# Performance work log

Measured on AMD Instinct MI355X. Metric: run time of the kernel, lower is better.

## Reference

```python
import jax, jax.numpy as jnp
import numpy as np

N_NODES = 100000
N_EDGES = 1600000
IN_DIM, HID_DIM, OUT_DIM = 384, 64, 64
DROP_P = 0.5


def setup_inputs() -> dict:
    key = jax.random.key(0)
    ks = jax.random.split(key, 9)
    x = jax.random.normal(ks[0], (N_NODES, IN_DIM), dtype=jnp.float32)
    edge_index = jax.random.randint(ks[1], (2, N_EDGES), 0, N_NODES, dtype=jnp.int64)
    edge_weight = jax.random.uniform(ks[2], (N_EDGES,), dtype=jnp.float32)
    W1 = jax.random.normal(ks[3], (IN_DIM, HID_DIM), dtype=jnp.float32) * (1.0 / np.sqrt(IN_DIM))
    b1 = jnp.zeros((HID_DIM,), dtype=jnp.float32)
    W2 = jax.random.normal(ks[4], (HID_DIM, OUT_DIM), dtype=jnp.float32) * (1.0 / np.sqrt(HID_DIM))
    b2 = jnp.zeros((OUT_DIM,), dtype=jnp.float32)
    drop_mask1 = jax.random.bernoulli(ks[5], 1.0 - DROP_P, (N_NODES, IN_DIM))
    drop_mask2 = jax.random.bernoulli(ks[6], 1.0 - DROP_P, (N_NODES, HID_DIM))
    return {"x": x, "edge_index": edge_index, "edge_weight": edge_weight,
            "W1": W1, "b1": b1, "W2": W2, "b2": b2,
            "drop_mask1": drop_mask1, "drop_mask2": drop_mask2}


def _gcn_conv(h, W, b, src, dst, edge_weight, n_nodes):
    # GCNConv: linear transform first (smaller dim), then normalized sparse aggregation
    h = h @ W                                        # [N, d_out]
    msg = h[src] * edge_weight[:, None]              # gather over edges [E, d_out]
    agg = jax.ops.segment_sum(msg, dst, num_segments=n_nodes)  # scatter-add [N, d_out]
    return agg + b


def reference(x, edge_index, edge_weight, W1, b1, W2, b2, drop_mask1, drop_mask2):
    scale = 1.0 / (1.0 - DROP_P)
    src, dst = edge_index[0], edge_index[1]
    n = x.shape[0]
    h = x * drop_mask1.astype(x.dtype) * scale                  # dropout (training)
    h = jax.nn.relu(_gcn_conv(h, W1, b1, src, dst, edge_weight, n))
    h = h * drop_mask2.astype(h.dtype) * scale                  # dropout (training)
    return _gcn_conv(h, W2, b2, src, dst, edge_weight, n)
```

## Files before the change

kernel.cpp:

```cpp
#include <hip/hip_runtime.h>
#include <hip/hip_bf16.h>
#include <stdint.h>

#define N_NODES 100000
#define N_EDGES 1600000
#define IN_DIM  384
#define HID_DIM 64
#define SCAN_NB 391

typedef __attribute__((ext_vector_type(8))) short short8_t;
typedef __attribute__((ext_vector_type(4))) float f32x4;

__global__ void k_detect(const uint32_t* __restrict__ ei,
                         const uint32_t* __restrict__ m1,
                         int* __restrict__ flags) {
    int l = threadIdx.x;
    uint32_t hi = ei[2 * l + 1];
    int ei64 = __all(hi == 0u);

    uint32_t maxb = 0;
    int bf = 0, f16 = 0, hib = 0;
    for (int i = 0; i < 4; ++i) {
        uint32_t w = m1[l * 4 + i];
        uint32_t b0 = w & 0xffu, b1 = (w >> 8) & 0xffu,
                 b2 = (w >> 16) & 0xffu, b3 = (w >> 24) & 0xffu;
        uint32_t mb = b0 > b1 ? b0 : b1;
        uint32_t mb2 = b2 > b3 ? b2 : b3;
        mb = mb > mb2 ? mb : mb2;
        maxb = maxb > mb ? maxb : mb;
        if ((w & 0xffffu) == 0x3f80u) bf = 1;
        if ((w & 0xffffu) == 0x3c00u) f16 = 1;
        if ((b1 | b2 | b3) != 0u) hib = 1;
    }
    int small  = __all(maxb <= 1u);
    int anybf  = __any(bf);
    int anyf16 = __any(f16);
    int anyhib = __any(hib);
    if (l == 0) {
        flags[0] = ei64;
        int mm;
        if (small)                 mm = anyhib ? 3 : 4;
        else if (anybf || anyf16)  mm = 0;
        else                       mm = 2;
        flags[1] = mm;
    }
}

__device__ __forceinline__ float mask_at(const void* p, int mode, long idx) {
    if (mode == 0) return ((const uint16_t*)p)[idx] ? 2.0f : 0.0f;
    if (mode == 2) return ((const float*)p)[idx] != 0.0f ? 2.0f : 0.0f;
    if (mode == 3) return ((const uint8_t*)p)[idx] ? 2.0f : 0.0f;
    return ((const int*)p)[idx] ? 2.0f : 0.0f;
}

__device__ __forceinline__ void load_edge(const int* p32, int mode64, long e,
                                          int& s, int& d) {
    if (mode64) { s = p32[2 * e]; d = p32[2 * (N_EDGES + e)]; }
    else        { s = p32[e];     d = p32[N_EDGES + e]; }
}

__device__ __forceinline__ ushort f2bf(float f) {
    uint32_t u = __float_as_uint(f);
    return (ushort)((u + 0x7fffu + ((u >> 16) & 1u)) >> 16);
}
__device__ __forceinline__ float bf2f(ushort h) {
    return __uint_as_float(((uint32_t)h) << 16);
}

__global__ __launch_bounds__(256) void k_hist(const void* __restrict__ ei,
                                              uint32_t* __restrict__ deg,
                                              const int* __restrict__ flags) {
    const int mode64 = flags[0];
    const int* p32 = (const int*)ei;
    for (long e = (long)blockIdx.x * 256 + threadIdx.x; e < N_EDGES;
         e += (long)gridDim.x * 256) {
        int s, d; load_edge(p32, mode64, e, s, d);
        atomicAdd(&deg[d], 1u);
    }
}

__global__ __launch_bounds__(256) void k_scanA(const uint32_t* __restrict__ deg,
                                               uint32_t* __restrict__ partials) {
    __shared__ uint32_t sbuf[256];
    int idx = blockIdx.x * 256 + threadIdx.x;
    uint32_t v = idx < N_NODES ? deg[idx] : 0u;
    sbuf[threadIdx.x] = v;
    __syncthreads();
    for (int off = 128; off > 0; off >>= 1) {
        if (threadIdx.x < off) sbuf[threadIdx.x] += sbuf[threadIdx.x + off];
        __syncthreads();
    }
    if (threadIdx.x == 0) partials[blockIdx.x] = sbuf[0];
}

__global__ __launch_bounds__(512) void k_scanB(const uint32_t* __restrict__ partials,
                                               uint32_t* __restrict__ poff,
                                               uint32_t* __restrict__ starts) {
    __shared__ uint32_t sbuf[512];
    int t = threadIdx.x;
    uint32_t v = t < SCAN_NB ? partials[t] : 0u;
    sbuf[t] = v;
    __syncthreads();
    for (int off = 1; off < 512; off <<= 1) {
        uint32_t add = t >= off ? sbuf[t - off] : 0u;
        __syncthreads();
        sbuf[t] += add;
        __syncthreads();
    }
    if (t < SCAN_NB) poff[t] = sbuf[t] - v;
    if (t == SCAN_NB - 1) starts[N_NODES] = sbuf[t];
}

__global__ __launch_bounds__(256) void k_scanC(const uint32_t* __restrict__ deg,
                                               const uint32_t* __restrict__ poff,
                                               uint32_t* __restrict__ starts) {
    __shared__ uint32_t sbuf[256];
    int idx = blockIdx.x * 256 + threadIdx.x;
    uint32_t v = idx < N_NODES ? deg[idx] : 0u;
    sbuf[threadIdx.x] = v;
    __syncthreads();
    for (int off = 1; off < 256; off <<= 1) {
        uint32_t add = threadIdx.x >= off ? sbuf[threadIdx.x - off] : 0u;
        __syncthreads();
        sbuf[threadIdx.x] += add;
        __syncthreads();
    }
    if (idx < N_NODES) starts[idx] = poff[blockIdx.x] + sbuf[threadIdx.x] - v;
}

__global__ __launch_bounds__(256) void k_reorder(const void* __restrict__ ei,
                                                 const float* __restrict__ ew,
                                                 uint32_t* __restrict__ cursors,
                                                 int2* __restrict__ sorted,
                                                 const int* __restrict__ flags) {
    const int mode64 = flags[0];
    const int* p32 = (const int*)ei;
    for (long e = (long)blockIdx.x * 256 + threadIdx.x; e < N_EDGES;
         e += (long)gridDim.x * 256) {
        int s, d; load_edge(p32, mode64, e, s, d);
        float w = ew[e];
        uint32_t pos = atomicAdd(&cursors[d], 1u);
        sorted[pos] = make_int2(s, __float_as_int(w));
    }
}

__global__ __launch_bounds__(256) void k_packW(const float* __restrict__ W1,
                                               ushort* __restrict__ Wpack) {
    const int ks = blockIdx.x;
    const int t  = threadIdx.x;
    const int nt = t >> 6, l = t & 63;
    ushort hs[8], ls[8];
#pragma unroll
    for (int j = 0; j < 8; ++j) {
        float wv = W1[(ks * 32 + (l >> 4) * 8 + j) * 64 + nt * 16 + (l & 15)];
        ushort h = f2bf(wv);
        hs[j] = h;
        ls[j] = f2bf(wv - bf2f(h));
    }
    *(short8_t*)&Wpack[((8 * ks + nt) * 64 + l) * 8]     = *(short8_t*)hs;
    *(short8_t*)&Wpack[((8 * ks + 4 + nt) * 64 + l) * 8] = *(short8_t*)ls;
}

__global__ __launch_bounds__(256) void k1_mfma(
        const float* __restrict__ x, const void* __restrict__ m1,
        const ushort* __restrict__ Wpack, ushort* __restrict__ Hb,
        const int* __restrict__ flags) {
    const int mmode = flags[1];
    const int t = threadIdx.x;
    const int l = t & 63, w = t >> 6;
    const int node0 = blockIdx.x * 64;
    const long row = node0 + w * 16 + (l & 15);
    const int kq = (l >> 4) * 8;
    const bool valid = row < N_NODES;

    f32x4 acc[4];
#pragma unroll
    for (int i = 0; i < 4; ++i) acc[i] = (f32x4)0.0f;

    for (int ks = 0; ks < 12; ++ks) {
        float xv[8];
        if (valid) {
            long gb = row * IN_DIM + ks * 32 + kq;
            float4 x0 = *(const float4*)(x + gb);
            float4 x1 = *(const float4*)(x + gb + 4);
            xv[0] = x0.x; xv[1] = x0.y; xv[2] = x0.z; xv[3] = x0.w;
            xv[4] = x1.x; xv[5] = x1.y; xv[6] = x1.z; xv[7] = x1.w;
            float mv[8];
            if (mmode == 0) {
                const ushort* mp = (const ushort*)m1 + gb;
                ushort4 a = *(const ushort4*)mp;
                ushort4 b = *(const ushort4*)(mp + 4);
                mv[0] = a.x ? 2.f : 0.f; mv[1] = a.y ? 2.f : 0.f;
                mv[2] = a.z ? 2.f : 0.f; mv[3] = a.w ? 2.f : 0.f;
                mv[4] = b.x ? 2.f : 0.f; mv[5] = b.y ? 2.f : 0.f;
                mv[6] = b.z ? 2.f : 0.f; mv[7] = b.w ? 2.f : 0.f;
            } else if (mmode == 2) {
                const float* mp = (const float*)m1 + gb;
                float4 a = *(const float4*)mp;
                float4 b = *(const float4*)(mp + 4);
                mv[0] = a.x != 0.f ? 2.f : 0.f; mv[1] = a.y != 0.f ? 2.f : 0.f;
                mv[2] = a.z != 0.f ? 2.f : 0.f; mv[3] = a.w != 0.f ? 2.f : 0.f;
                mv[4] = b.x != 0.f ? 2.f : 0.f; mv[5] = b.y != 0.f ? 2.f : 0.f;
                mv[6] = b.z != 0.f ? 2.f : 0.f; mv[7] = b.w != 0.f ? 2.f : 0.f;
            } else if (mmode == 3) {
                uint2 mb = *(const uint2*)((const uint8_t*)m1 + gb);
#pragma unroll
                for (int j = 0; j < 4; ++j) {
                    mv[j]     = ((mb.x >> (8 * j)) & 0xffu) ? 2.f : 0.f;
                    mv[4 + j] = ((mb.y >> (8 * j)) & 0xffu) ? 2.f : 0.f;
                }
            } else {
                const int* mp = (const int*)m1 + gb;
                int4 a = *(const int4*)mp;
                int4 b = *(const int4*)(mp + 4);
                mv[0] = a.x ? 2.f : 0.f; mv[1] = a.y ? 2.f : 0.f;
                mv[2] = a.z ? 2.f : 0.f; mv[3] = a.w ? 2.f : 0.f;
                mv[4] = b.x ? 2.f : 0.f; mv[5] = b.y ? 2.f : 0.f;
                mv[6] = b.z ? 2.f : 0.f; mv[7] = b.w ? 2.f : 0.f;
            }
#pragma unroll
            for (int j = 0; j < 8; ++j) xv[j] *= mv[j];
        } else {
#pragma unroll
            for (int j = 0; j < 8; ++j) xv[j] = 0.0f;
        }
        ushort ap[8];
#pragma unroll
        for (int j = 0; j < 8; ++j) ap[j] = f2bf(xv[j]);
        short8_t ah = *(short8_t*)ap;

#pragma unroll
        for (int nt = 0; nt < 4; ++nt) {
            short8_t bh = *(const short8_t*)&Wpack[((8 * ks + nt) * 64 + l) * 8];
            short8_t bl = *(const short8_t*)&Wpack[((8 * ks + 4 + nt) * 64 + l) * 8];
            acc[nt] = __builtin_amdgcn_mfma_f32_16x16x32_bf16(ah, bh, acc[nt], 0, 0, 0);
            acc[nt] = __builtin_amdgcn_mfma_f32_16x16x32_bf16(ah, bl, acc[nt], 0, 0, 0);
        }
    }
    const int r0 = (l >> 4) * 4;
#pragma unroll
    for (int nt = 0; nt < 4; ++nt) {
#pragma unroll
        for (int r = 0; r < 4; ++r) {
            long node = node0 + w * 16 + r0 + r;
            if (node < N_NODES)
                Hb[node * 64 + nt * 16 + (l & 15)] = f2bf(acc[nt][r]);
        }
    }
}

__global__ __launch_bounds__(256) void k_aggmlp(
        const ushort* __restrict__ Hb, const int2* __restrict__ sorted,
        const uint32_t* __restrict__ starts, const float* __restrict__ b1,
        const void* __restrict__ m2, const float* __restrict__ W2,
        ushort* __restrict__ H2b, const int* __restrict__ flags) {
    __shared__ float w2s[64 * 64];
    __shared__ float vbuf[4][64];
    const int mmode = flags[1];
    for (int i = threadIdx.x; i < 4096; i += 256) w2s[i] = W2[i];
    __syncthreads();

    const int lane = threadIdx.x & 63;
    const int w = threadIdx.x >> 6;
    const long n = (long)blockIdx.x * 4 + w;
    uint32_t e  = starts[n];
    uint32_t e1 = starts[n + 1];
    float acc = 0.0f;
    for (; e + 4 <= e1; e += 4) {
        int2 p0 = sorted[e],     p1 = sorted[e + 1];
        int2 p2 = sorted[e + 2], p3 = sorted[e + 3];
        float v0 = bf2f(Hb[(long)p0.x * 64 + lane]);
        float v1 = bf2f(Hb[(long)p1.x * 64 + lane]);
        float v2 = bf2f(Hb[(long)p2.x * 64 + lane]);
        float v3 = bf2f(Hb[(long)p3.x * 64 + lane]);
        acc = fmaf(v0, __int_as_float(p0.y), acc);
        acc = fmaf(v1, __int_as_float(p1.y), acc);
        acc = fmaf(v2, __int_as_float(p2.y), acc);
        acc = fmaf(v3, __int_as_float(p3.y), acc);
    }
    for (; e < e1; ++e) {
        int2 p0 = sorted[e];
        acc = fmaf(bf2f(Hb[(long)p0.x * 64 + lane]), __int_as_float(p0.y), acc);
    }
    float u = acc + b1[lane];
    u = u > 0.0f ? u : 0.0f;
    u *= mask_at(m2, mmode, n * 64 + lane);
    vbuf[w][lane] = u;
    float h2 = 0.0f;
#pragma unroll
    for (int j = 0; j < 64; j += 4) {
        float4 v4 = *(const float4*)&vbuf[w][j];
        h2 = fmaf(v4.x, w2s[(j + 0) * 64 + lane], h2);
        h2 = fmaf(v4.y, w2s[(j + 1) * 64 + lane], h2);
        h2 = fmaf(v4.z, w2s[(j + 2) * 64 + lane], h2);
        h2 = fmaf(v4.w, w2s[(j + 3) * 64 + lane], h2);
    }
    H2b[n * 64 + lane] = f2bf(h2);
}

__global__ __launch_bounds__(256) void k_agg(const ushort* __restrict__ Hb,
                                             const int2* __restrict__ sorted,
                                             const uint32_t* __restrict__ starts,
                                             const float* __restrict__ bias,
                                             float* __restrict__ dest) {
    const int lane = threadIdx.x & 63;
    const long n = (long)blockIdx.x * 4 + (threadIdx.x >> 6);
    if (n >= N_NODES) return;
    uint32_t e  = starts[n];
    uint32_t e1 = starts[n + 1];
    float acc = bias[lane];
    for (; e + 4 <= e1; e += 4) {
        int2 p0 = sorted[e],     p1 = sorted[e + 1];
        int2 p2 = sorted[e + 2], p3 = sorted[e + 3];
        float v0 = bf2f(Hb[(long)p0.x * 64 + lane]);
        float v1 = bf2f(Hb[(long)p1.x * 64 + lane]);
        float v2 = bf2f(Hb[(long)p2.x * 64 + lane]);
        float v3 = bf2f(Hb[(long)p3.x * 64 + lane]);
        acc = fmaf(v0, __int_as_float(p0.y), acc);
        acc = fmaf(v1, __int_as_float(p1.y), acc);
        acc = fmaf(v2, __int_as_float(p2.y), acc);
        acc = fmaf(v3, __int_as_float(p3.y), acc);
    }
    for (; e < e1; ++e) {
        int2 p0 = sorted[e];
        acc = fmaf(bf2f(Hb[(long)p0.x * 64 + lane]), __int_as_float(p0.y), acc);
    }
    dest[n * 64 + lane] = acc;
}

__global__ __launch_bounds__(256) void k_scatter(
        const ushort* __restrict__ Hb, const void* __restrict__ ei,
        const float* __restrict__ ew, float* __restrict__ dest,
        const int* __restrict__ flags) {
    const int mode64 = flags[0];
    const int lane = threadIdx.x & 63;
    const long wid = (long)blockIdx.x * 4 + (threadIdx.x >> 6);
    const long nw = (long)gridDim.x * 4;
    const int* p32 = (const int*)ei;
    for (long e = wid; e < N_EDGES; e += nw) {
        int s, d; load_edge(p32, mode64, e, s, d);
        float w = ew[e];
        float v = bf2f(Hb[(long)s * 64 + lane]) * w;
        atomicAdd(&dest[(long)d * 64 + lane], v);
    }
}

__global__ __launch_bounds__(256) void k3_mlp(
        const float* __restrict__ agg, const float* __restrict__ b1,
        const void* __restrict__ m2, const float* __restrict__ W2,
        ushort* __restrict__ H2b, const int* __restrict__ flags) {
    __shared__ float w2s[64 * 64];
    __shared__ float vbuf[4][64];
    const int mmode = flags[1];
    for (int i = threadIdx.x; i < 4096; i += 256) w2s[i] = W2[i];
    __syncthreads();
    const int lane = threadIdx.x & 63;
    const int w = threadIdx.x >> 6;
    const float bc = b1[lane];
    const long wid = (long)blockIdx.x * 4 + w;
    const long nw = (long)gridDim.x * 4;
    for (long n = wid; n < N_NODES; n += nw) {
        float u = agg[n * 64 + lane] + bc;
        u = u > 0.0f ? u : 0.0f;
        u *= mask_at(m2, mmode, n * 64 + lane);
        vbuf[w][lane] = u;
        float acc = 0.0f;
#pragma unroll
        for (int j = 0; j < 64; j += 4) {
            float4 v4 = *(const float4*)&vbuf[w][j];
            acc = fmaf(v4.x, w2s[(j + 0) * 64 + lane], acc);
            acc = fmaf(v4.y, w2s[(j + 1) * 64 + lane], acc);
            acc = fmaf(v4.z, w2s[(j + 2) * 64 + lane], acc);
            acc = fmaf(v4.w, w2s[(j + 3) * 64 + lane], acc);
        }
        H2b[n * 64 + lane] = f2bf(acc);
    }
}

__global__ void k_init_out(float* __restrict__ out, const float* __restrict__ b2) {
    const long total = (long)N_NODES * 16;
    for (long j = (long)blockIdx.x * 256 + threadIdx.x; j < total;
         j += (long)gridDim.x * 256) {
        ((float4*)out)[j] = ((const float4*)b2)[j & 15];
    }
}

extern "C" void kernel_launch(void* const* d_in, const int* in_sizes, int n_in,
                              void* d_out, int out_size, void* d_ws, size_t ws_size,
                              hipStream_t stream) {
    const float* x  = (const float*)d_in[0];
    const void*  ei = d_in[1];
    const float* ew = (const float*)d_in[2];
    const float* W1 = (const float*)d_in[3];
    const float* b1 = (const float*)d_in[4];
    const float* W2 = (const float*)d_in[5];
    const float* b2 = (const float*)d_in[6];
    const void*  m1 = d_in[7];
    const void*  m2 = d_in[8];
    float* out = (float*)d_out;

    char* ws = (char*)d_ws;
    size_t off = 0;
    auto alloc = [&](size_t bytes) {
        char* p = ws + off;
        off += (bytes + 255) & ~(size_t)255;
        return p;
    };
    int*      flags   = (int*)alloc(32);
    ushort*   Hb      = (ushort*)alloc((size_t)N_NODES * 64 * 2);
    ushort*   H2b     = (ushort*)alloc((size_t)N_NODES * 64 * 2);
    float*    AGG     = (float*)alloc((size_t)N_NODES * 64 * 4);
    int2*     sorted  = (int2*)alloc((size_t)N_EDGES * 8);
    uint32_t* starts  = (uint32_t*)alloc((size_t)(N_NODES + 1) * 4);
    uint32_t* deg     = (uint32_t*)alloc((size_t)N_NODES * 4);
    uint32_t* cursors = (uint32_t*)alloc((size_t)N_NODES * 4);
    uint32_t* poff    = (uint32_t*)alloc((size_t)SCAN_NB * 4);
    ushort*   Wpack   = (ushort*)alloc((size_t)12 * 8 * 64 * 8 * 2);
    size_t need = off;

    hipLaunchKernelGGL(k_detect, dim3(1), dim3(64), 0, stream,
                       (const uint32_t*)ei, (const uint32_t*)m1, flags);
    hipLaunchKernelGGL(k_packW, dim3(12), dim3(256), 0, stream, W1, Wpack);

    if (ws_size >= need) {
        hipMemsetAsync(deg, 0, (size_t)N_NODES * 4, stream);
        hipLaunchKernelGGL(k_hist, dim3(2048), dim3(256), 0, stream,
                           ei, deg, flags);
        hipLaunchKernelGGL(k_scanA, dim3(SCAN_NB), dim3(256), 0, stream,
                           deg, poff);
        hipLaunchKernelGGL(k_scanB, dim3(1), dim3(512), 0, stream,
                           poff, cursors, starts);
        hipLaunchKernelGGL(k_scanC, dim3(SCAN_NB), dim3(256), 0, stream,
                           deg, cursors, starts);
        hipMemcpyAsync(cursors, starts, (size_t)N_NODES * 4,
                       hipMemcpyDeviceToDevice, stream);
        hipLaunchKernelGGL(k_reorder, dim3(2048), dim3(256), 0, stream,
                           ei, ew, cursors, sorted, flags);
        hipLaunchKernelGGL(k1_mfma, dim3((N_NODES + 63) / 64), dim3(256), 0, stream,
                           x, m1, Wpack, Hb, flags);
        hipLaunchKernelGGL(k_aggmlp, dim3(N_NODES / 4), dim3(256), 0, stream,
                           Hb, sorted, starts, b1, m2, W2, H2b, flags);
        hipLaunchKernelGGL(k_agg, dim3(N_NODES / 4), dim3(256), 0, stream,
                           H2b, sorted, starts, b2, out);
    } else {
        hipMemsetAsync(AGG, 0, (size_t)N_NODES * 64 * 4, stream);
        hipLaunchKernelGGL(k1_mfma, dim3((N_NODES + 63) / 64), dim3(256), 0, stream,
                           x, m1, Wpack, Hb, flags);
        hipLaunchKernelGGL(k_scatter, dim3(4096), dim3(256), 0, stream,
                           Hb, ei, ew, AGG, flags);
        hipLaunchKernelGGL(k3_mlp, dim3(1024), dim3(256), 0, stream,
                           AGG, b1, m2, W2, H2b, flags);
        hipLaunchKernelGGL(k_init_out, dim3(2048), dim3(256), 0, stream, out, b2);
        hipLaunchKernelGGL(k_scatter, dim3(4096), dim3(256), 0, stream,
                           H2b, ei, ew, out, flags);
    }
}
```

Before: 785.3 us.

## Partition degree histogram and CSR cursors into eight copies to cut atomic contention

Edges are binned into eight per-partition histograms and cursor arrays, chosen by block index. The scan runs over the combined partition-major array and also writes the cursors directly, which drops the device-to-device memcpy. Each aggregation now walks eight short segments per node and loads sixteen start offsets, with a 2-way unroll instead of 4. This lowers contention on the histogram and reorder atomics, at the cost of scattered small segments and extra index loads in the gather kernels. The CSR buffers now share workspace with the unused fallback AGG buffer.

Result: slower. 855.9 us (+9.0%).

```diff
diff --git a/kernel.cpp b/kernel.cpp
--- a/kernel.cpp
+++ b/kernel.cpp
@@ -6,7 +6,10 @@
 #define N_EDGES 1600000
 #define IN_DIM  384
 #define HID_DIM 64
-#define SCAN_NB 391
+#define NPART   8
+#define NP      (NPART * N_NODES)
+#define SCAN8_NB 782
+#define EGRID   2048
 
 typedef __attribute__((ext_vector_type(8))) short short8_t;
 typedef __attribute__((ext_vector_type(4))) float f32x4;
@@ -67,24 +70,31 @@
     return __uint_as_float(((uint32_t)h) << 16);
 }
 
-__global__ __launch_bounds__(256) void k_hist(const void* __restrict__ ei,
-                                              uint32_t* __restrict__ deg,
-                                              const int* __restrict__ flags) {
+__global__ __launch_bounds__(256) void k_hist8(const void* __restrict__ ei,
+                                               uint32_t* __restrict__ deg8,
+                                               const int* __restrict__ flags) {
     const int mode64 = flags[0];
     const int* p32 = (const int*)ei;
+    const long pbase = (long)(blockIdx.x & (NPART - 1)) * N_NODES;
     for (long e = (long)blockIdx.x * 256 + threadIdx.x; e < N_EDGES;
-         e += (long)gridDim.x * 256) {
+         e += (long)EGRID * 256) {
         int s, d; load_edge(p32, mode64, e, s, d);
-        atomicAdd(&deg[d], 1u);
-    }
-}
-
-__global__ __launch_bounds__(256) void k_scanA(const uint32_t* __restrict__ deg,
-                                               uint32_t* __restrict__ partials) {
+        atomicAdd(&deg8[pbase + d], 1u);
+    }
+}
+
+__global__ __launch_bounds__(256) void k_scanA8(const uint32_t* __restrict__ deg,
+                                                uint32_t* __restrict__ partials) {
     __shared__ uint32_t sbuf[256];
-    int idx = blockIdx.x * 256 + threadIdx.x;
-    uint32_t v = idx < N_NODES ? deg[idx] : 0u;
-    sbuf[threadIdx.x] = v;
+    long base = (long)blockIdx.x * 1024 + threadIdx.x * 4;
+    uint32_t s = 0;
+    if (base + 3 < NP) {
+        uint4 v = *(const uint4*)&deg[base];
+        s = v.x + v.y + v.z + v.w;
+    } else {
+        for (int j = 0; j < 4; ++j) if (base + j < NP) s += deg[base + j];
+    }
+    sbuf[threadIdx.x] = s;
     __syncthreads();
     for (int off = 128; off > 0; off >>= 1) {
         if (threadIdx.x < off) sbuf[threadIdx.x] += sbuf[threadIdx.x + off];
@@ -93,31 +103,39 @@
     if (threadIdx.x == 0) partials[blockIdx.x] = sbuf[0];
 }
 
-__global__ __launch_bounds__(512) void k_scanB(const uint32_t* __restrict__ partials,
-                                               uint32_t* __restrict__ poff,
-                                               uint32_t* __restrict__ starts) {
-    __shared__ uint32_t sbuf[512];
+__global__ __launch_bounds__(1024) void k_scanB8(const uint32_t* __restrict__ partials,
+                                                 uint32_t* __restrict__ poff,
+                                                 uint32_t* __restrict__ starts) {
+    __shared__ uint32_t sbuf[1024];
     int t = threadIdx.x;
-    uint32_t v = t < SCAN_NB ? partials[t] : 0u;
+    uint32_t v = t < SCAN8_NB ? partials[t] : 0u;
     sbuf[t] = v;
     __syncthreads();
-    for (int off = 1; off < 512; off <<= 1) {
+    for (int off = 1; off < 1024; off <<= 1) {
         uint32_t add = t >= off ? sbuf[t - off] : 0u;
         __syncthreads();
         sbuf[t] += add;
         __syncthreads();
     }
-    if (t < SCAN_NB) poff[t] = sbuf[t] - v;
-    if (t == SCAN_NB - 1) starts[N_NODES] = sbuf[t];
-}
-
-__global__ __launch_bounds__(256) void k_scanC(const uint32_t* __restrict__ deg,
-                                               const uint32_t* __restrict__ poff,
-                                               uint32_t* __restrict__ starts) {
+    if (t < SCAN8_NB) poff[t] = sbuf[t] - v;
+    if (t == SCAN8_NB - 1) starts[NP] = sbuf[t];
+}
+
+__global__ __launch_bounds__(256) void k_scanC8(const uint32_t* __restrict__ deg,
+                                                const uint32_t* __restrict__ poff,
+                                                uint32_t* __restrict__ starts,
+                                                uint32_t* __restrict__ cur) {
     __shared__ uint32_t sbuf[256];
-    int idx = blockIdx.x * 256 + threadIdx.x;
-    uint32_t v = idx < N_NODES ? deg[idx] : 0u;
-    sbuf[threadIdx.x] = v;
+    long base = (long)blockIdx.x * 1024 + threadIdx.x * 4;
+    uint32_t v[4] = {0, 0, 0, 0};
+    if (base + 3 < NP) {
+        uint4 q = *(const uint4*)&deg[base];
+        v[0] = q.x; v[1] = q.y; v[2] = q.z; v[3] = q.w;
+    } else {
+        for (int j = 0; j < 4; ++j) if (base + j < NP) v[j] = deg[base + j];
+    }
+    uint32_t ts = v[0] + v[1] + v[2] + v[3];
+    sbuf[threadIdx.x] = ts;
     __syncthreads();
     for (int off = 1; off < 256; off <<= 1) {
         uint32_t add = threadIdx.x >= off ? sbuf[threadIdx.x - off] : 0u;
@@ -125,21 +143,29 @@
         sbuf[threadIdx.x] += add;
         __syncthreads();
     }
-    if (idx < N_NODES) starts[idx] = poff[blockIdx.x] + sbuf[threadIdx.x] - v;
-}
-
-__global__ __launch_bounds__(256) void k_reorder(const void* __restrict__ ei,
-                                                 const float* __restrict__ ew,
-                                                 uint32_t* __restrict__ cursors,
-                                                 int2* __restrict__ sorted,
-                                                 const int* __restrict__ flags) {
+    uint32_t run = poff[blockIdx.x] + sbuf[threadIdx.x] - ts;
+    for (int j = 0; j < 4; ++j) {
+        if (base + j < NP) {
+            starts[base + j] = run;
+            cur[base + j]    = run;
+            run += v[j];
+        }
+    }
+}
+
+__global__ __launch_bounds__(256) void k_reorder8(const void* __restrict__ ei,
+                                                  const float* __restrict__ ew,
+                                                  uint32_t* __restrict__ cur8,
+                                                  int2* __restrict__ sorted,
+                                                  const int* __restrict__ flags) {
     const int mode64 = flags[0];
     const int* p32 = (const int*)ei;
+    const long pbase = (long)(blockIdx.x & (NPART - 1)) * N_NODES;
     for (long e = (long)blockIdx.x * 256 + threadIdx.x; e < N_EDGES;
-         e += (long)gridDim.x * 256) {
+         e += (long)EGRID * 256) {
         int s, d; load_edge(p32, mode64, e, s, d);
         float w = ew[e];
-        uint32_t pos = atomicAdd(&cursors[d], 1u);
+        uint32_t pos = atomicAdd(&cur8[pbase + d], 1u);
         sorted[pos] = make_int2(s, __float_as_int(w));
     }
 }
@@ -249,6 +275,31 @@
     }
 }
 
+__device__ __forceinline__ float agg_node(const ushort* __restrict__ Hb,
+                                          const int2* __restrict__ sorted,
+                                          const uint32_t* __restrict__ starts,
+                                          int n, int lane) {
+    float acc = 0.0f;
+#pragma unroll 1
+    for (int p = 0; p < NPART; ++p) {
+        uint32_t e  = starts[p * N_NODES + n];
+        uint32_t e1 = starts[p * N_NODES + n + 1];
+        for (; e + 2 <= e1; e += 2) {
+            int2 p0 = sorted[e];
+            int2 p1 = sorted[e + 1];
+            float v0 = bf2f(Hb[(long)p0.x * 64 + lane]);
+            float v1 = bf2f(Hb[(long)p1.x * 64 + lane]);
+            acc = fmaf(v0, __int_as_float(p0.y), acc);
+            acc = fmaf(v1, __int_as_float(p1.y), acc);
+        }
+        if (e < e1) {
+            int2 p0 = sorted[e];
+            acc = fmaf(bf2f(Hb[(long)p0.x * 64 + lane]), __int_as_float(p0.y), acc);
+        }
+    }
+    return acc;
+}
+
 __global__ __launch_bounds__(256) void k_aggmlp(
         const ushort* __restrict__ Hb, const int2* __restrict__ sorted,
         const uint32_t* __restrict__ starts, const float* __restrict__ b1,
@@ -262,29 +313,11 @@
 
     const int lane = threadIdx.x & 63;
     const int w = threadIdx.x >> 6;
-    const long n = (long)blockIdx.x * 4 + w;
-    uint32_t e  = starts[n];
-    uint32_t e1 = starts[n + 1];
-    float acc = 0.0f;
-    for (; e + 4 <= e1; e += 4) {
-        int2 p0 = sorted[e],     p1 = sorted[e + 1];
-        int2 p2 = sorted[e + 2], p3 = sorted[e + 3];
-        float v0 = bf2f(Hb[(long)p0.x * 64 + lane]);
-        float v1 = bf2f(Hb[(long)p1.x * 64 + lane]);
-        float v2 = bf2f(Hb[(long)p2.x * 64 + lane]);
-        float v3 = bf2f(Hb[(long)p3.x * 64 + lane]);
-        acc = fmaf(v0, __int_as_float(p0.y), acc);
-        acc = fmaf(v1, __int_as_float(p1.y), acc);
-        acc = fmaf(v2, __int_as_float(p2.y), acc);
-        acc = fmaf(v3, __int_as_float(p3.y), acc);
-    }
-    for (; e < e1; ++e) {
-        int2 p0 = sorted[e];
-        acc = fmaf(bf2f(Hb[(long)p0.x * 64 + lane]), __int_as_float(p0.y), acc);
-    }
+    const int n = blockIdx.x * 4 + w;
+    float acc = agg_node(Hb, sorted, starts, n, lane);
     float u = acc + b1[lane];
     u = u > 0.0f ? u : 0.0f;
-    u *= mask_at(m2, mmode, n * 64 + lane);
+    u *= mask_at(m2, mmode, (long)n * 64 + lane);
     vbuf[w][lane] = u;
     float h2 = 0.0f;
 #pragma unroll
@@ -295,7 +328,7 @@
         h2 = fmaf(v4.z, w2s[(j + 2) * 64 + lane], h2);
         h2 = fmaf(v4.w, w2s[(j + 3) * 64 + lane], h2);
     }
-    H2b[n * 64 + lane] = f2bf(h2);
+    H2b[(long)n * 64 + lane] = f2bf(h2);
 }
 
 __global__ __launch_bounds__(256) void k_agg(const ushort* __restrict__ Hb,
@@ -304,28 +337,10 @@
                                              const float* __restrict__ bias,
                                              float* __restrict__ dest) {
     const int lane = threadIdx.x & 63;
-    const long n = (long)blockIdx.x * 4 + (threadIdx.x >> 6);
+    const int n = blockIdx.x * 4 + (threadIdx.x >> 6);
     if (n >= N_NODES) return;
-    uint32_t e  = starts[n];
-    uint32_t e1 = starts[n + 1];
-    float acc = bias[lane];
-    for (; e + 4 <= e1; e += 4) {
-        int2 p0 = sorted[e],     p1 = sorted[e + 1];
-        int2 p2 = sorted[e + 2], p3 = sorted[e + 3];
-        float v0 = bf2f(Hb[(long)p0.x * 64 + lane]);
-        float v1 = bf2f(Hb[(long)p1.x * 64 + lane]);
-        float v2 = bf2f(Hb[(long)p2.x * 64 + lane]);
-        float v3 = bf2f(Hb[(long)p3.x * 64 + lane]);
-        acc = fmaf(v0, __int_as_float(p0.y), acc);
-        acc = fmaf(v1, __int_as_float(p1.y), acc);
-        acc = fmaf(v2, __int_as_float(p2.y), acc);
-        acc = fmaf(v3, __int_as_float(p3.y), acc);
-    }
-    for (; e < e1; ++e) {
-        int2 p0 = sorted[e];
-        acc = fmaf(bf2f(Hb[(long)p0.x * 64 + lane]), __int_as_float(p0.y), acc);
-    }
-    dest[n * 64 + lane] = acc;
+    float acc = bias[lane] + agg_node(Hb, sorted, starts, n, lane);
+    dest[(long)n * 64 + lane] = acc;
 }
 
 __global__ __launch_bounds__(256) void k_scatter(
@@ -406,16 +421,18 @@
         off += (bytes + 255) & ~(size_t)255;
         return p;
     };
-    int*      flags   = (int*)alloc(32);
-    ushort*   Hb      = (ushort*)alloc((size_t)N_NODES * 64 * 2);
-    ushort*   H2b     = (ushort*)alloc((size_t)N_NODES * 64 * 2);
-    float*    AGG     = (float*)alloc((size_t)N_NODES * 64 * 4);
-    int2*     sorted  = (int2*)alloc((size_t)N_EDGES * 8);
-    uint32_t* starts  = (uint32_t*)alloc((size_t)(N_NODES + 1) * 4);
-    uint32_t* deg     = (uint32_t*)alloc((size_t)N_NODES * 4);
-    uint32_t* cursors = (uint32_t*)alloc((size_t)N_NODES * 4);
-    uint32_t* poff    = (uint32_t*)alloc((size_t)SCAN_NB * 4);
-    ushort*   Wpack   = (ushort*)alloc((size_t)12 * 8 * 64 * 8 * 2);
+    int*    flags = (int*)alloc(32);
+    ushort* Hb    = (ushort*)alloc((size_t)N_NODES * 64 * 2);
+    ushort* H2b   = (ushort*)alloc((size_t)N_NODES * 64 * 2);
+    char*   region = alloc((size_t)N_NODES * 64 * 4);
+    int2*     sorted = (int2*)region;
+    uint32_t* starts = (uint32_t*)(region + (size_t)N_EDGES * 8);
+    uint32_t* cur8   = starts + (NP + 64);
+    uint32_t* deg8   = cur8 + NP;
+    float*    AGG    = (float*)region;
+    uint32_t* partials = (uint32_t*)alloc((size_t)SCAN8_NB * 4);
+    uint32_t* poff     = (uint32_t*)alloc((size_t)SCAN8_NB * 4);
+    ushort*   Wpack    = (ushort*)alloc((size_t)12 * 8 * 64 * 8 * 2);
     size_t need = off;
 
     hipLaunchKernelGGL(k_detect, dim3(1), dim3(64), 0, stream,
@@ -423,19 +440,17 @@
     hipLaunchKernelGGL(k_packW, dim3(12), dim3(256), 0, stream, W1, Wpack);
 
     if (ws_size >= need) {
-        hipMemsetAsync(deg, 0, (size_t)N_NODES * 4, stream);
-        hipLaunchKernelGGL(k_hist, dim3(2048), dim3(256), 0, stream,
-                           ei, deg, flags);
-        hipLaunchKernelGGL(k_scanA, dim3(SCAN_NB), dim3(256), 0, stream,
-                           deg, poff);
-        hipLaunchKernelGGL(k_scanB, dim3(1), dim3(512), 0, stream,
-                           poff, cursors, starts);
-        hipLaunchKernelGGL(k_scanC, dim3(SCAN_NB), dim3(256), 0, stream,
-                           deg, cursors, starts);
-        hipMemcpyAsync(cursors, starts, (size_t)N_NODES * 4,
-                       hipMemcpyDeviceToDevice, stream);
-        hipLaunchKernelGGL(k_reorder, dim3(2048), dim3(256), 0, stream,
-                           ei, ew, cursors, sorted, flags);
+        hipMemsetAsync(deg8, 0, (size_t)NP * 4, stream);
+        hipLaunchKernelGGL(k_hist8, dim3(EGRID), dim3(256), 0, stream,
+                           ei, deg8, flags);
+        hipLaunchKernelGGL(k_scanA8, dim3(SCAN8_NB), dim3(256), 0, stream,
+                           deg8, partials);
+        hipLaunchKernelGGL(k_scanB8, dim3(1), dim3(1024), 0, stream,
+                           partials, poff, starts);
+        hipLaunchKernelGGL(k_scanC8, dim3(SCAN8_NB), dim3(256), 0, stream,
+                           deg8, poff, starts, cur8);
+        hipLaunchKernelGGL(k_reorder8, dim3(EGRID), dim3(256), 0, stream,
+                           ei, ew, cur8, sorted, flags);
         hipLaunchKernelGGL(k1_mfma, dim3((N_NODES + 63) / 64), dim3(256), 0, stream,
                            x, m1, Wpack, Hb, flags);
         hipLaunchKernelGGL(k_aggmlp, dim3(N_NODES / 4), dim3(256), 0, stream,
```
